# Kernel tuning notes

Hardware: AMD Instinct MI355X
Metric: run time of the kernel (lower is better)

## Reference

```python
import jax, jax.numpy as jnp
import numpy as np

N_NODES = 50000
N_EDGES = 800000
DIM = 128
LN_EPS = 1e-5


def setup_inputs() -> dict:
    key = jax.random.key(0)
    k1, k2, k3, k4 = jax.random.split(key, 4)
    h = jax.random.normal(k1, (N_NODES, DIM), dtype=jnp.float32)
    edge_index = jax.random.randint(k2, (2, N_EDGES), 0, N_NODES, dtype=jnp.int64)
    W = jax.random.normal(k3, (DIM, DIM), dtype=jnp.float32) / np.sqrt(DIM)
    b = jnp.zeros((DIM,), dtype=jnp.float32)
    gamma = jnp.ones((DIM,), dtype=jnp.float32)
    beta = jnp.zeros((DIM,), dtype=jnp.float32)
    t = jnp.zeros((), dtype=jnp.float32)
    return {"t": t, "h": h, "edge_index": edge_index, "batch_size": N_NODES,
            "W": W, "b": b, "gamma": gamma, "beta": beta}


def _gcn_conv(h, edge_index, W, b):
    """PyG-style GCNConv: D^{-1/2} (A+I) D^{-1/2} (h W) + b."""
    N = h.shape[0]
    loops = jnp.arange(N, dtype=edge_index.dtype)
    src = jnp.concatenate([edge_index[0], loops])  # [E+N]
    dst = jnp.concatenate([edge_index[1], loops])  # [E+N]
    # degree (with self loops) on destination nodes
    deg = jax.ops.segment_sum(jnp.ones_like(dst, dtype=h.dtype), dst, num_segments=N)
    dinv = jnp.where(deg > 0, jax.lax.rsqrt(deg), 0.0)
    norm = dinv[src] * dinv[dst]                    # [E+N]
    xw = h @ W                                      # [N, D]
    msg = xw[src] * norm[:, None]                   # gather + scale, [E+N, D]
    agg = jax.ops.segment_sum(msg, dst, num_segments=N)  # scatter-add, [N, D]
    return agg + b


def reference(t, h, edge_index, batch_size, W, b, gamma, beta):
    if h.ndim == 1:
        h = h[None, :]
    dh = _gcn_conv(h, edge_index, W, b)
    # LayerNorm over feature dim, then tanh
    mean = jnp.mean(dh, axis=-1, keepdims=True)
    var = jnp.mean(jnp.square(dh - mean), axis=-1, keepdims=True)
    dh = (dh - mean) * jax.lax.rsqrt(var + LN_EPS) * gamma + beta
    dh = jnp.tanh(dh)
    return (dh, jnp.zeros_like(edge_index), jnp.zeros_like(jnp.asarray(batch_size)))
```

## Files before the change

### kernel.cpp

```cpp
#include <hip/hip_runtime.h>
#include <math.h>

#define NN 50000
#define NE 800000
#define D  128
#define PG_BLOCKS 782
#define NROLES 1564
#define SC_BLOCKS 782

typedef __attribute__((ext_vector_type(8))) short bf16x8;
typedef __attribute__((ext_vector_type(4))) float f32x4;

__device__ __forceinline__ unsigned short f32_to_bf16(float f) {
    unsigned u = __float_as_uint(f);
    u = u + 0x7FFFu + ((u >> 16) & 1u);
    return (unsigned short)(u >> 16);
}

__device__ __forceinline__ float fast_tanh(float x) {
    float e = __expf(2.0f * x);
    return fmaf(-2.0f, __builtin_amdgcn_rcpf(e + 1.0f), 1.0f);
}

#define GLD16(P, VO, BASE)                                              \
    asm volatile(                                                       \
        "global_load_dword %0, %16, %32\n\t"                            \
        "global_load_dword %1, %17, %32\n\t"                            \
        "global_load_dword %2, %18, %32\n\t"                            \
        "global_load_dword %3, %19, %32\n\t"                            \
        "global_load_dword %4, %20, %32\n\t"                            \
        "global_load_dword %5, %21, %32\n\t"                            \
        "global_load_dword %6, %22, %32\n\t"                            \
        "global_load_dword %7, %23, %32\n\t"                            \
        "global_load_dword %8, %24, %32\n\t"                            \
        "global_load_dword %9, %25, %32\n\t"                            \
        "global_load_dword %10, %26, %32\n\t"                           \
        "global_load_dword %11, %27, %32\n\t"                           \
        "global_load_dword %12, %28, %32\n\t"                           \
        "global_load_dword %13, %29, %32\n\t"                           \
        "global_load_dword %14, %30, %32\n\t"                           \
        "global_load_dword %15, %31, %32\n\t"                           \
        "s_waitcnt vmcnt(0)"                                            \
        : "=&v"(P[0]),  "=&v"(P[1]),  "=&v"(P[2]),  "=&v"(P[3]),        \
          "=&v"(P[4]),  "=&v"(P[5]),  "=&v"(P[6]),  "=&v"(P[7]),        \
          "=&v"(P[8]),  "=&v"(P[9]),  "=&v"(P[10]), "=&v"(P[11]),       \
          "=&v"(P[12]), "=&v"(P[13]), "=&v"(P[14]), "=&v"(P[15])        \
        : "v"(VO[0]),  "v"(VO[1]),  "v"(VO[2]),  "v"(VO[3]),            \
          "v"(VO[4]),  "v"(VO[5]),  "v"(VO[6]),  "v"(VO[7]),            \
          "v"(VO[8]),  "v"(VO[9]),  "v"(VO[10]), "v"(VO[11]),           \
          "v"(VO[12]), "v"(VO[13]), "v"(VO[14]), "v"(VO[15]),           \
          "s"(BASE))

__global__ __launch_bounds__(256) void k_init(
        const float* __restrict__ Wg, int* __restrict__ deg,
        unsigned short* __restrict__ wpk, unsigned short* __restrict__ zb) {
    int tid = threadIdx.x;
    int idx = blockIdx.x * 256 + tid;

    if (idx < NN / 4) ((int4*)deg)[idx] = (int4){0, 0, 0, 0};

    if (blockIdx.x == 0) {
#pragma unroll 8
        for (int i = 0; i < 64; i++) {
            int o = i * 256 + tid;
            int j = o & 7, frag = o >> 3;
            int lo = frag & 15, quad = (frag >> 4) & 3;
            int kt = (frag >> 6) & 3, nt = frag >> 8;
            wpk[o] = f32_to_bf16(Wg[(kt * 32 + quad * 8 + j) * 128 + nt * 16 + lo]);
        }
    }
    if (blockIdx.x == 1 && tid < 64)
        ((unsigned*)(zb + (size_t)NN * D))[tid] = 0u;
}

__global__ __launch_bounds__(256) void k_count_gemm(
        const float* __restrict__ h, const uint4* __restrict__ wpk4,
        const int* __restrict__ ei, int* __restrict__ deg,
        int* __restrict__ ell, float* __restrict__ zf,
        int* __restrict__ outtail, int tailN) {
    int tid = threadIdx.x;
    int bid = blockIdx.x;

    if (bid & 1) {
        int g = (bid >> 1) * 256 + tid;
        if (g < NE / 4) {
            int4 s4 = ((const int4*)ei)[g];
            int4 d4 = ((const int4*)(ei + NE))[g];
            int rx = atomicAdd(&deg[d4.x], 1);
            int ry = atomicAdd(&deg[d4.y], 1);
            int rz = atomicAdd(&deg[d4.z], 1);
            int rw = atomicAdd(&deg[d4.w], 1);
            if (rx < 64) ell[(size_t)d4.x * 64 + rx] = s4.x;
            if (ry < 64) ell[(size_t)d4.y * 64 + ry] = s4.y;
            if (rz < 64) ell[(size_t)d4.z * 64 + rz] = s4.z;
            if (rw < 64) ell[(size_t)d4.w * 64 + rw] = s4.w;
        }
        for (int i = g; i < tailN; i += PG_BLOCKS * 256) outtail[i] = 0;
        return;
    }

    int gid = bid >> 1;
    int w = tid >> 6, lane = tid & 63;
    int quad = lane >> 4, lo = lane & 15;
    int rowBase = gid * 64 + w * 16;
    int rowA = rowBase + lo; if (rowA > NN - 1) rowA = NN - 1;
    const float4* h4 = (const float4*)h;

    bf16x8 af[4];
#pragma unroll
    for (int kt = 0; kt < 4; kt++) {
        float4 u = h4[(size_t)rowA * 32 + kt * 8 + quad * 2];
        float4 v = h4[(size_t)rowA * 32 + kt * 8 + quad * 2 + 1];
        bf16x8 a;
        a[0] = (short)f32_to_bf16(u.x); a[1] = (short)f32_to_bf16(u.y);
        a[2] = (short)f32_to_bf16(u.z); a[3] = (short)f32_to_bf16(u.w);
        a[4] = (short)f32_to_bf16(v.x); a[5] = (short)f32_to_bf16(v.y);
        a[6] = (short)f32_to_bf16(v.z); a[7] = (short)f32_to_bf16(v.w);
        af[kt] = a;
    }

    f32x4 acc[8];
#pragma unroll
    for (int nt = 0; nt < 8; nt++) acc[nt] = (f32x4){0.f, 0.f, 0.f, 0.f};

#pragma unroll
    for (int kt = 0; kt < 4; kt++)
#pragma unroll
        for (int nt = 0; nt < 8; nt++) {
            uint4 tb = wpk4[nt * 256 + kt * 64 + lane];
            acc[nt] = __builtin_amdgcn_mfma_f32_16x16x32_bf16(
                af[kt], __builtin_bit_cast(bf16x8, tb), acc[nt], 0, 0, 0);
        }

#pragma unroll
    for (int reg = 0; reg < 4; reg++) {
        int row = rowBase + quad * 4 + reg;
        if (row < NN) {
#pragma unroll
            for (int nt = 0; nt < 8; nt++)
                zf[(size_t)row * D + nt * 16 + lo] = acc[nt][reg];
        }
    }
}

__global__ __launch_bounds__(256) void k_scale(
        const int* __restrict__ deg, const float* __restrict__ zf,
        unsigned short* __restrict__ zb) {
    int g = blockIdx.x * 256 + threadIdx.x;
    if (g < NN * 4) {
        int row = g >> 2, seg = g & 3;
        float dn = rsqrtf((float)deg[row] + 1.0f);
        const float4* src = (const float4*)(zf + (size_t)row * D + seg * 32);
        uint4* dst = (uint4*)(zb + (size_t)row * D + seg * 32);
#pragma unroll
        for (int i = 0; i < 4; i++) {
            float4 a = src[i * 2], bb = src[i * 2 + 1];
            uint4 o;
            o.x = (unsigned)f32_to_bf16(a.x * dn) | ((unsigned)f32_to_bf16(a.y * dn) << 16);
            o.y = (unsigned)f32_to_bf16(a.z * dn) | ((unsigned)f32_to_bf16(a.w * dn) << 16);
            o.z = (unsigned)f32_to_bf16(bb.x * dn) | ((unsigned)f32_to_bf16(bb.y * dn) << 16);
            o.w = (unsigned)f32_to_bf16(bb.z * dn) | ((unsigned)f32_to_bf16(bb.w * dn) << 16);
            dst[i] = o;
        }
    }
}

__global__ __launch_bounds__(256) void k_gather_ln(
        const int* __restrict__ deg, const int* __restrict__ ell,
        const unsigned* __restrict__ zbu,
        const float* __restrict__ bias, const float* __restrict__ gamma,
        const float* __restrict__ beta, float* __restrict__ out) {
    int tid = threadIdx.x;
    int w = tid >> 6, lane = tid & 63;
    int rowBase = blockIdx.x * 16 + w * 4;
    unsigned lane4 = (unsigned)(lane << 2);

    int m0[4]; float dn[4]; unsigned selfz[4]; int v[4];
#pragma unroll
    for (int r = 0; r < 4; r++) {
        int row = rowBase + r;
        int dg = __builtin_amdgcn_readfirstlane(deg[row]);
        dn[r] = rsqrtf((float)dg + 1.0f);
        m0[r] = (dg > 64) ? 64 : dg;
        selfz[r] = zbu[(size_t)row * 64 + lane];
        int t0 = ell[(size_t)row * 64 + lane];
        v[r] = (lane < m0[r]) ? t0 : NN;
    }

    float ax[4], ay[4];
#pragma unroll
    for (int r = 0; r < 4; r++) {
        ax[r] = __uint_as_float(selfz[r] << 16);
        ay[r] = __uint_as_float(selfz[r] & 0xFFFF0000u);
    }

    float2 x[4];
#pragma unroll
    for (int r = 0; r < 4; r++) {
        int nb = (m0[r] + 15) >> 4;
        for (int jb = 0; jb < nb; ++jb) {
            int j = jb << 4;
            unsigned vo[16], p[16];
#pragma unroll
            for (int q = 0; q < 16; q++) {
                int sq = __builtin_amdgcn_readlane(v[r], j + q);
                vo[q] = ((unsigned)sq << 8) + lane4;
            }
            GLD16(p, vo, zbu);
#pragma unroll
            for (int q = 0; q < 16; q++) {
                ax[r] += __uint_as_float(p[q] << 16);
                ay[r] += __uint_as_float(p[q] & 0xFFFF0000u);
            }
        }
        x[r].x = ax[r] * dn[r];
        x[r].y = ay[r] * dn[r];
    }

    float2 bi = ((const float2*)bias)[lane];
    float2 ga = ((const float2*)gamma)[lane];
    float2 be = ((const float2*)beta)[lane];
#pragma unroll
    for (int r = 0; r < 4; r++) {
        int row = rowBase + r;
        float y0 = x[r].x + bi.x;
        float y1 = x[r].y + bi.y;
        float s = y0 + y1;
#pragma unroll
        for (int off = 32; off > 0; off >>= 1) s += __shfl_xor(s, off, 64);
        float m = s * (1.0f / 128.0f);
        float v0f = y0 - m, v1f = y1 - m;
        float vs = v0f * v0f + v1f * v1f;
#pragma unroll
        for (int off = 32; off > 0; off >>= 1) vs += __shfl_xor(vs, off, 64);
        float rstd = rsqrtf(vs * (1.0f / 128.0f) + 1e-5f);
        float2 o;
        o.x = fast_tanh(v0f * rstd * ga.x + be.x);
        o.y = fast_tanh(v1f * rstd * ga.y + be.y);
        *(float2*)&out[(size_t)row * D + lane * 2] = o;
    }
}

extern "C" void kernel_launch(void* const* d_in, const int* in_sizes, int n_in,
                              void* d_out, int out_size, void* d_ws, size_t ws_size,
                              hipStream_t stream) {
    const float* h     = (const float*)d_in[1];
    const int*   ei    = (const int*)  d_in[2];
    const float* Wg    = (const float*)d_in[4];
    const float* b     = (const float*)d_in[5];
    const float* gamma = (const float*)d_in[6];
    const float* beta  = (const float*)d_in[7];
    float* out = (float*)d_out;

    char* wsb = (char*)d_ws;
    unsigned short* wpk = (unsigned short*)(wsb);
    int*            deg = (int*)(wsb + 32768);
    int*            ell = (int*)(wsb + 232768);
    unsigned short* zb  = (unsigned short*)(wsb + 13032768);
    float*          zf  = (float*)(wsb + 25833024);

    int tailN = out_size - NN * D;
    int* outtail = (int*)(out + (size_t)NN * D);

    k_init       <<<64,        256, 0, stream>>>(Wg, deg, wpk, zb);
    k_count_gemm <<<NROLES,    256, 0, stream>>>(h, (const uint4*)wpk, ei, deg, ell, zf, outtail, tailN);
    k_scale      <<<SC_BLOCKS, 256, 0, stream>>>(deg, zf, zb);
    k_gather_ln  <<<NN / 16,   256, 0, stream>>>(deg, ell, (const unsigned*)zb, b, gamma, beta, out);
}
```

Before: 188.4 us.

## Store ELL neighbor indices as 16-bit and rebalance count/GEMM block roles

Neighbor indices in the ELL table are stored as unsigned short instead of int, which halves the ELL footprint and the bytes moved in both the scatter and the gather kernels. Degree-count blocks now handle 8 edges per thread and run as a separate block range ahead of the GEMM blocks, rather than being interleaved one-for-one with them. The output tail zeroing is spread across all blocks and uses int4 stores. Node ids above 65535 would be truncated, and N=50000 still fits.

Measured after the change: 197.1 us. +4.6%, slower.

```diff
diff --git a/kernel.cpp b/kernel.cpp
--- a/kernel.cpp
+++ b/kernel.cpp
@@ -4,8 +4,9 @@
 #define NN 50000
 #define NE 800000
 #define D  128
-#define PG_BLOCKS 782
-#define NROLES 1564
+#define CNT_BLOCKS 391
+#define GEMM_BLOCKS 782
+#define NROLES (CNT_BLOCKS + GEMM_BLOCKS)
 #define SC_BLOCKS 782
 
 typedef __attribute__((ext_vector_type(8))) short bf16x8;
@@ -76,30 +77,48 @@
 __global__ __launch_bounds__(256) void k_count_gemm(
         const float* __restrict__ h, const uint4* __restrict__ wpk4,
         const int* __restrict__ ei, int* __restrict__ deg,
-        int* __restrict__ ell, float* __restrict__ zf,
+        unsigned short* __restrict__ ell, float* __restrict__ zf,
         int* __restrict__ outtail, int tailN) {
     int tid = threadIdx.x;
     int bid = blockIdx.x;
 
-    if (bid & 1) {
-        int g = (bid >> 1) * 256 + tid;
-        if (g < NE / 4) {
-            int4 s4 = ((const int4*)ei)[g];
-            int4 d4 = ((const int4*)(ei + NE))[g];
-            int rx = atomicAdd(&deg[d4.x], 1);
-            int ry = atomicAdd(&deg[d4.y], 1);
-            int rz = atomicAdd(&deg[d4.z], 1);
-            int rw = atomicAdd(&deg[d4.w], 1);
-            if (rx < 64) ell[(size_t)d4.x * 64 + rx] = s4.x;
-            if (ry < 64) ell[(size_t)d4.y * 64 + ry] = s4.y;
-            if (rz < 64) ell[(size_t)d4.z * 64 + rz] = s4.z;
-            if (rw < 64) ell[(size_t)d4.w * 64 + rw] = s4.w;
-        }
-        for (int i = g; i < tailN; i += PG_BLOCKS * 256) outtail[i] = 0;
+    {
+        int gt = bid * 256 + tid;
+        int tail4 = tailN >> 2;
+        for (int i = gt; i < tail4; i += NROLES * 256)
+            ((int4*)outtail)[i] = (int4){0, 0, 0, 0};
+        if (gt == 0)
+            for (int k2 = tail4 << 2; k2 < tailN; k2++) outtail[k2] = 0;
+    }
+
+    if (bid < CNT_BLOCKS) {
+        int g = bid * 256 + tid;
+        if (g < NE / 8) {
+            int4 sa = ((const int4*)ei)[2 * g];
+            int4 sb = ((const int4*)ei)[2 * g + 1];
+            int4 da = ((const int4*)(ei + NE))[2 * g];
+            int4 db = ((const int4*)(ei + NE))[2 * g + 1];
+            int r0 = atomicAdd(&deg[da.x], 1);
+            int r1 = atomicAdd(&deg[da.y], 1);
+            int r2 = atomicAdd(&deg[da.z], 1);
+            int r3 = atomicAdd(&deg[da.w], 1);
+            int r4 = atomicAdd(&deg[db.x], 1);
+            int r5 = atomicAdd(&deg[db.y], 1);
+            int r6 = atomicAdd(&deg[db.z], 1);
+            int r7 = atomicAdd(&deg[db.w], 1);
+            if (r0 < 64) ell[(size_t)da.x * 64 + r0] = (unsigned short)sa.x;
+            if (r1 < 64) ell[(size_t)da.y * 64 + r1] = (unsigned short)sa.y;
+            if (r2 < 64) ell[(size_t)da.z * 64 + r2] = (unsigned short)sa.z;
+            if (r3 < 64) ell[(size_t)da.w * 64 + r3] = (unsigned short)sa.w;
+            if (r4 < 64) ell[(size_t)db.x * 64 + r4] = (unsigned short)sb.x;
+            if (r5 < 64) ell[(size_t)db.y * 64 + r5] = (unsigned short)sb.y;
+            if (r6 < 64) ell[(size_t)db.z * 64 + r6] = (unsigned short)sb.z;
+            if (r7 < 64) ell[(size_t)db.w * 64 + r7] = (unsigned short)sb.w;
+        }
         return;
     }
 
-    int gid = bid >> 1;
+    int gid = bid - CNT_BLOCKS;
     int w = tid >> 6, lane = tid & 63;
     int quad = lane >> 4, lo = lane & 15;
     int rowBase = gid * 64 + w * 16;
@@ -166,7 +185,7 @@
 }
 
 __global__ __launch_bounds__(256) void k_gather_ln(
-        const int* __restrict__ deg, const int* __restrict__ ell,
+        const int* __restrict__ deg, const unsigned short* __restrict__ ell,
         const unsigned* __restrict__ zbu,
         const float* __restrict__ bias, const float* __restrict__ gamma,
         const float* __restrict__ beta, float* __restrict__ out) {
@@ -183,7 +202,7 @@
         dn[r] = rsqrtf((float)dg + 1.0f);
         m0[r] = (dg > 64) ? 64 : dg;
         selfz[r] = zbu[(size_t)row * 64 + lane];
-        int t0 = ell[(size_t)row * 64 + lane];
+        int t0 = (int)ell[(size_t)row * 64 + lane];
         v[r] = (lane < m0[r]) ? t0 : NN;
     }
 
@@ -255,9 +274,9 @@
     char* wsb = (char*)d_ws;
     unsigned short* wpk = (unsigned short*)(wsb);
     int*            deg = (int*)(wsb + 32768);
-    int*            ell = (int*)(wsb + 232768);
-    unsigned short* zb  = (unsigned short*)(wsb + 13032768);
-    float*          zf  = (float*)(wsb + 25833024);
+    unsigned short* ell = (unsigned short*)(wsb + 232768);
+    unsigned short* zb  = (unsigned short*)(wsb + 6632768);
+    float*          zf  = (float*)(wsb + 19433024);
 
     int tailN = out_size - NN * D;
     int* outtail = (int*)(out + (size_t)NN * D);
```
